# Kernel optimization log

Hardware: AMD Instinct MI355X
Metric: run time of the kernel (lower is better)

The kernel has to match this reference:

```python
import jax, jax.numpy as jnp
import numpy as np

HIDDEN = 1024
HEADS = 16
HEAD_DIM = HIDDEN // HEADS


def setup_inputs() -> dict:
    key = jax.random.key(0)
    ks = jax.random.split(key, 7)
    B, S = 2, 2048
    scale = 1.0 / np.sqrt(HIDDEN)
    return {
        "hidden_states": jax.random.normal(ks[0], (B, S, HIDDEN), dtype=jnp.float32),
        "attention_mask": jnp.zeros((B, S), dtype=jnp.float32),
        "Wq": jax.random.normal(ks[1], (HIDDEN, HIDDEN), dtype=jnp.float32) * scale,
        "bq": jnp.zeros((HIDDEN,), dtype=jnp.float32),
        "Wk": jax.random.normal(ks[2], (HIDDEN, HIDDEN), dtype=jnp.float32) * scale,
        "bk": jnp.zeros((HIDDEN,), dtype=jnp.float32),
        "Wv": jax.random.normal(ks[3], (HIDDEN, HIDDEN), dtype=jnp.float32) * scale,
        "bv": jnp.zeros((HIDDEN,), dtype=jnp.float32),
    }


def reference(hidden_states, attention_mask, Wq, bq, Wk, bk, Wv, bv):
    B, S, _ = hidden_states.shape
    def heads(x):  # [B,S,HIDDEN] -> [B,H,S,D]
        return x.reshape(B, S, HEADS, HEAD_DIM).transpose(0, 2, 1, 3)
    q = heads(hidden_states @ Wq + bq)
    k = heads(hidden_states @ Wk + bk)
    v = heads(hidden_states @ Wv + bv)
    scores = jnp.einsum('bhqd,bhkd->bhqk', q, k) / np.sqrt(HEAD_DIM).astype(np.float32)
    # additive mask broadcast [B,1,1,S]
    scores = scores + attention_mask[:, None, None, :]
    probs = jax.nn.softmax(scores, axis=-1)
    # dropout is identity in eval mode (reference baseline)
    ctx = jnp.einsum('bhqk,bhkd->bhqd', probs, v)
    return ctx.transpose(0, 2, 1, 3).reshape(B, S, HIDDEN)
```

## Files before the change

kernel.cpp:

```cpp
#include <hip/hip_runtime.h>
#include <cstdint>
#include <cstddef>

typedef __bf16 bf16;
typedef _Float16 f16;
typedef __attribute__((ext_vector_type(8))) __bf16 bf16x8;
typedef __attribute__((ext_vector_type(4))) float f32x4;
typedef __attribute__((ext_vector_type(16))) float f32x16;
typedef __attribute__((ext_vector_type(4))) _Float16 f16x4;
typedef __attribute__((ext_vector_type(8))) _Float16 f16x8;

#define MFMA16(a, b, c) __builtin_amdgcn_mfma_f32_16x16x32_bf16((a), (b), (c), 0, 0, 0)
#define MFMA32(a, b, c) __builtin_amdgcn_mfma_f32_32x32x16_bf16((a), (b), (c), 0, 0, 0)

static constexpr int BB   = 2;
static constexpr int SS   = 2048;
static constexpr int HID  = 1024;
static constexpr int NH   = 16;
static constexpr int HD   = 64;
static constexpr int MROW = BB * SS;
static constexpr int NQKV = 3 * HID;
static constexpr float LOG2E = 1.4426950408889634f;
static constexpr float MSHIFT = 16.0f;

__device__ __forceinline__ int SW(int r) { return ((r ^ (r >> 3)) & 7) << 4; }

__device__ __forceinline__ uint32_t pack_bf16(float a, float b) {
    union { bf16 h[2]; uint32_t u; } x;
    x.h[0] = (bf16)a; x.h[1] = (bf16)b;
    return x.u;
}

__device__ __forceinline__ uint32_t pack_raw(bf16 a, bf16 b) {
    union { bf16 h[2]; uint32_t u; } x;
    x.h[0] = a; x.h[1] = b;
    return x.u;
}

__device__ __forceinline__ float exp2i(float x) {
    float r; asm("v_exp_f32 %0, %1" : "=v"(r) : "v"(x)); return r;
}

__device__ __forceinline__ void plswap(uint32_t& a, uint32_t& b) {
    asm("v_permlane32_swap_b32 %0, %1" : "+v"(a), "+v"(b));
}

__device__ __forceinline__ void gload16(const void* g, void* l) {
    __builtin_amdgcn_global_load_lds(
        (const __attribute__((address_space(1))) void*)g,
        (__attribute__((address_space(3))) void*)l, 16, 0, 0);
}

__global__ __launch_bounds__(256) void cvt_hidden(const float* __restrict__ in,
                                                  bf16* __restrict__ out) {
    const int i = (blockIdx.x * 256 + threadIdx.x) * 8;
    float4 f0 = *(const float4*)&in[i];
    float4 f1 = *(const float4*)&in[i + 4];
    bf16x8 o;
    o[0] = (bf16)f0.x; o[1] = (bf16)f0.y; o[2] = (bf16)f0.z; o[3] = (bf16)f0.w;
    o[4] = (bf16)f1.x; o[5] = (bf16)f1.y; o[6] = (bf16)f1.z; o[7] = (bf16)f1.w;
    *(bf16x8*)&out[i] = o;
}

__global__ __launch_bounds__(256) void maskcvt(const float* __restrict__ m,
                                               float* __restrict__ o) {
    const int i = blockIdx.x * 256 + threadIdx.x;
    o[i] = m[i] * LOG2E - MSHIFT;
}

__global__ __launch_bounds__(256) void wtrans(const float* __restrict__ Wq,
                                              const float* __restrict__ Wk,
                                              const float* __restrict__ Wv,
                                              bf16* __restrict__ Wt) {
    __shared__ float tile[32][33];
    const float* W = (blockIdx.z == 0) ? Wq : (blockIdx.z == 1) ? Wk : Wv;
    bf16* O = Wt + (size_t)blockIdx.z * HID * HID;
    const int x  = blockIdx.x * 32 + threadIdx.x;
    const int y0 = blockIdx.y * 32;
#pragma unroll
    for (int i = threadIdx.y; i < 32; i += 8)
        tile[i][threadIdx.x] = W[(size_t)(y0 + i) * HID + x];
    __syncthreads();
    const int k = y0 + threadIdx.x;
#pragma unroll
    for (int i = threadIdx.y; i < 32; i += 8)
        O[(size_t)(blockIdx.x * 32 + i) * HID + k] = (bf16)tile[threadIdx.x][i];
}

__global__ __launch_bounds__(256) void qkv_gemm(
    const bf16* __restrict__ A, const bf16* __restrict__ Bt,
    const float* __restrict__ bq, const float* __restrict__ bk,
    const float* __restrict__ bv,
    bf16* __restrict__ Qo, bf16* __restrict__ Ko, bf16* __restrict__ Vo) {
    __shared__ __align__(16) bf16 As[128 * 32];
    __shared__ __align__(16) bf16 Bs[128 * 32];
    const int t = threadIdx.x, l = t & 63;
    const int l15 = l & 15, l4 = l >> 4;
    const int w = t >> 6;
    const int wm = w >> 1, wn = w & 1;
    const int m0 = blockIdx.y * 128, n0 = blockIdx.x * 128;

    f32x4 acc[4][4] = {};

    for (int kt = 0; kt < 32; ++kt) {
        const int k0 = kt * 32;
        __syncthreads();
#pragma unroll
        for (int cc = 0; cc < 2; ++cc) {
            const int c = t + cc * 256;
            const int row = c >> 2, col = (c & 3) * 8;
            gload16(&A[(size_t)(m0 + row) * HID + k0 + col], (char*)As + c * 16);
            gload16(&Bt[(size_t)(n0 + row) * HID + k0 + col], (char*)Bs + c * 16);
        }
        __syncthreads();

        bf16x8 af[4], bf_[4];
#pragma unroll
        for (int mi = 0; mi < 4; ++mi) {
            const int r = wm * 64 + mi * 16 + l15;
            af[mi] = *(const bf16x8*)((const char*)As + r * 64 + l4 * 16);
        }
#pragma unroll
        for (int ni = 0; ni < 4; ++ni) {
            const int r = wn * 64 + ni * 16 + l15;
            bf_[ni] = *(const bf16x8*)((const char*)Bs + r * 64 + l4 * 16);
        }
        __builtin_amdgcn_s_setprio(1);
#pragma unroll
        for (int mi = 0; mi < 4; ++mi)
#pragma unroll
            for (int ni = 0; ni < 4; ++ni)
                acc[mi][ni] = MFMA16(af[mi], bf_[ni], acc[mi][ni]);
        __builtin_amdgcn_s_setprio(0);
    }

#pragma unroll
    for (int mi = 0; mi < 4; ++mi) {
#pragma unroll
        for (int ni = 0; ni < 4; ++ni) {
            const int ng = n0 + wn * 64 + ni * 16 + l15;
            const int qkv = ng >> 10;
            const int nn = ng & 1023;
            const int hh = nn >> 6, dd = nn & 63;
            const float* bp = (qkv == 0) ? bq : (qkv == 1) ? bk : bv;
            bf16* op = (qkv == 0) ? Qo : (qkv == 1) ? Ko : Vo;
            const float bias = bp[nn];
            const float scl = (qkv == 0) ? 0.125f * LOG2E : 1.0f;
            const int mg = m0 + wm * 64 + mi * 16 + l4 * 4;
            const int bb = mg >> 11, ss = mg & 2047;
            bf16* dst = op + ((size_t)(bb * NH + hh) * SS + ss) * HD + dd;
#pragma unroll
            for (int j = 0; j < 4; ++j)
                dst[(size_t)j * HD] = (bf16)((acc[mi][ni][j] + bias) * scl);
        }
    }
}

__global__ __launch_bounds__(256) void attn_fwd(
    const bf16* __restrict__ Q, const bf16* __restrict__ K,
    const bf16* __restrict__ V, const float* __restrict__ mkl,
    f16* __restrict__ Op, float* __restrict__ ml) {
    __shared__ __align__(16) char Ks0[64 * 128];
    __shared__ __align__(16) char Ks1[64 * 128];
    __shared__ __align__(16) char Vt0[64 * 128];
    __shared__ __align__(16) char Vt1[64 * 128];

    const int t = threadIdx.x, l = t & 63, w = t >> 6;
    const int l31 = l & 31, h = l >> 5;

    const int bid = blockIdx.x;
    const int nid = (bid & 7) * 128 + (bid >> 3);
    const int bh = nid >> 5, kh = (nid >> 4) & 1, qb = nid & 15;
    const int q0 = qb * 128 + w * 32;
    const int kbase = kh * (SS / 2);

    const bf16* Qp = Q + (size_t)bh * SS * HD;
    const bf16* Kp = K + (size_t)bh * SS * HD;
    const bf16* Vp = V + (size_t)bh * SS * HD;
    const float* mkp = mkl + (bh >> 4) * SS;

    bf16x8 qf[4];
#pragma unroll
    for (int c = 0; c < 4; ++c)
        qf[c] = *(const bf16x8*)&Qp[(size_t)(q0 + l31) * HD + c * 16 + h * 8];

    bf16x8 ones;
#pragma unroll
    for (int i = 0; i < 8; ++i) ones[i] = (bf16)1.0f;

    f32x16 o0 = {}, o1 = {};
    f32x16 o2 = {};

    const int vp_ = t >> 3, vdb = (t & 7) * 8;

    auto stageK = [&](int tile, char* dst) {
        const int key0 = kbase + tile * 64;
#pragma unroll
        for (int cc = 0; cc < 2; ++cc) {
            const int c = t + cc * 256;
            const int row = c >> 3;
            const int csw = (c & 7) ^ ((row ^ (row >> 3)) & 7);
            gload16(&Kp[(size_t)(key0 + row) * HD + csw * 8], dst + c * 16);
        }
    };
    auto loadV = [&](int tile, bf16x8& va, bf16x8& vb) {
        const int key0 = kbase + tile * 64;
        va = *(const bf16x8*)&Vp[(size_t)(key0 + 2 * vp_) * HD + vdb];
        vb = *(const bf16x8*)&Vp[(size_t)(key0 + 2 * vp_ + 1) * HD + vdb];
    };
    auto storeV = [&](char* Vtn, const bf16x8& va, const bf16x8& vb) {
#pragma unroll
        for (int i = 0; i < 8; ++i) {
            const int d = vdb + i;
            *(uint32_t*)(Vtn + d * 128 + ((vp_ * 4) ^ SW(d))) =
                pack_raw(va[i], vb[i]);
        }
    };

    stageK(0, Ks0);
    {
        bf16x8 va, vb;
        loadV(0, va, vb);
        storeV(Vt0, va, vb);
    }
    __syncthreads();

    constexpr int NT = (SS / 2) / 64;
#pragma unroll 1
    for (int kt = 0; kt < NT; ++kt) {
        char* Ks = (kt & 1) ? Ks1 : Ks0;
        char* Vt = (kt & 1) ? Vt1 : Vt0;
        char* Ksn = (kt & 1) ? Ks0 : Ks1;
        char* Vtn = (kt & 1) ? Vt0 : Vt1;
        const int key0 = kbase + kt * 64;
        const bool more = (kt + 1) < NT;

        bf16x8 va = {}, vb = {};
        if (more) {
            stageK(kt + 1, Ksn);
            loadV(kt + 1, va, vb);
        }

        f32x16 s0, s1;
#pragma unroll
        for (int rq = 0; rq < 4; ++rq) {
            const f32x4 m0v = *(const f32x4*)&mkp[key0 + rq * 8 + 4 * h];
            const f32x4 m1v = *(const f32x4*)&mkp[key0 + 32 + rq * 8 + 4 * h];
#pragma unroll
            for (int j = 0; j < 4; ++j) {
                s0[rq * 4 + j] = m0v[j];
                s1[rq * 4 + j] = m1v[j];
            }
        }
        __builtin_amdgcn_s_setprio(1);
#pragma unroll
        for (int c = 0; c < 4; ++c) {
            const int r0 = l31;
            bf16x8 kf0 = *(const bf16x8*)(Ks + r0 * 128 +
                                          ((c * 32 + h * 16) ^ SW(r0)));
            s0 = MFMA32(kf0, qf[c], s0);
        }
#pragma unroll
        for (int c = 0; c < 4; ++c) {
            const int r1 = 32 + l31;
            bf16x8 kf1 = *(const bf16x8*)(Ks + r1 * 128 +
                                          ((c * 32 + h * 16) ^ SW(r1)));
            s1 = MFMA32(kf1, qf[c], s1);
        }
        __builtin_amdgcn_s_setprio(0);

#pragma unroll
        for (int g = 0; g < 2; ++g) {
            f32x16& st = g ? s1 : s0;
#pragma unroll
            for (int r = 0; r < 16; ++r) st[r] = exp2i(st[r]);
#pragma unroll
            for (int cc = 0; cc < 2; ++cc) {
                uint32_t wA = pack_bf16(st[8 * cc + 0], st[8 * cc + 1]);
                uint32_t wB = pack_bf16(st[8 * cc + 2], st[8 * cc + 3]);
                uint32_t wC = pack_bf16(st[8 * cc + 4], st[8 * cc + 5]);
                uint32_t wD = pack_bf16(st[8 * cc + 6], st[8 * cc + 7]);
                plswap(wA, wC);
                plswap(wB, wD);
                union { uint32_t u[4]; bf16x8 v; } pb;
                pb.u[0] = wA; pb.u[1] = wB; pb.u[2] = wC; pb.u[3] = wD;
                const int colb = g * 64 + cc * 32 + h * 16;
                __builtin_amdgcn_s_setprio(1);
                {
                    o2 = MFMA32(ones, pb.v, o2);
                    bf16x8 vf0 = *(const bf16x8*)(Vt + l31 * 128 +
                                                  (colb ^ SW(l31)));
                    o0 = MFMA32(vf0, pb.v, o0);
                    const int r1 = 32 + l31;
                    bf16x8 vf1 = *(const bf16x8*)(Vt + r1 * 128 +
                                                  (colb ^ SW(r1)));
                    o1 = MFMA32(vf1, pb.v, o1);
                }
                __builtin_amdgcn_s_setprio(0);
            }
            if (g == 0 && more) storeV(Vtn, va, vb);
        }
        __syncthreads();
    }

    const int part = kh * 512 + bh * 16 + qb;
    f16* Ob = Op + (size_t)part * 8192;
    const int row = w * 32 + l31;
#pragma unroll
    for (int rq = 0; rq < 4; ++rq) {
        f16x4 a, b2;
#pragma unroll
        for (int j = 0; j < 4; ++j) {
            a[j]  = (f16)o0[rq * 4 + j];
            b2[j] = (f16)o1[rq * 4 + j];
        }
        *(f16x4*)&Ob[row * 64 + rq * 8 + 4 * h] = a;
        *(f16x4*)&Ob[row * 64 + 32 + rq * 8 + 4 * h] = b2;
    }
    if (l < 32) ml[(size_t)part * 128 + (w * 32 + l)] = o2[0];
}

__global__ __launch_bounds__(256) void combine(
    const f16* __restrict__ Op, const float* __restrict__ ml,
    float* __restrict__ out) {
    const int tid = blockIdx.x * 256 + threadIdx.x;
    const int dg = tid & 7, gq = tid >> 3;
    const int bh = gq >> 11, s = gq & 2047;
    const int qb = s >> 7, q = s & 127;
    const int p0 = bh * 16 + qb, p1 = 512 + p0;

    const float l1 = ml[(size_t)p0 * 128 + q];
    const float l2 = ml[(size_t)p1 * 128 + q];
    const float inv = 1.0f / (l1 + l2);

    const f16x8 O1 = *(const f16x8*)&Op[(size_t)p0 * 8192 + q * 64 + dg * 8];
    const f16x8 O2 = *(const f16x8*)&Op[(size_t)p1 * 8192 + q * 64 + dg * 8];
    f32x4 r0, r1;
#pragma unroll
    for (int i = 0; i < 4; ++i) {
        r0[i] = ((float)O1[i] + (float)O2[i]) * inv;
        r1[i] = ((float)O1[4 + i] + (float)O2[4 + i]) * inv;
    }

    const int b = bh >> 4, hh = bh & 15;
    float* op = &out[((size_t)(b * SS + s)) * HID + hh * HD + dg * 8];
    *(f32x4*)op = r0;
    *(f32x4*)(op + 4) = r1;
}

extern "C" void kernel_launch(void* const* d_in, const int* in_sizes, int n_in,
                              void* d_out, int out_size, void* d_ws, size_t ws_size,
                              hipStream_t stream) {
    (void)in_sizes; (void)n_in; (void)out_size; (void)ws_size;
    const float* hs  = (const float*)d_in[0];
    const float* msk = (const float*)d_in[1];
    const float* Wq  = (const float*)d_in[2];
    const float* bq  = (const float*)d_in[3];
    const float* Wk  = (const float*)d_in[4];
    const float* bk  = (const float*)d_in[5];
    const float* Wv  = (const float*)d_in[6];
    const float* bv  = (const float*)d_in[7];
    float* out = (float*)d_out;
    char* ws = (char*)d_ws;
    const size_t MB = 1 << 20;

    bf16* Qb  = (bf16*)ws;
    bf16* Kb  = (bf16*)(ws + 8 * MB);
    bf16* Vb  = (bf16*)(ws + 16 * MB);
    float* mk2 = (float*)(ws + 24 * MB);
    bf16* Xb  = (bf16*)(ws + 25 * MB);
    bf16* Wt  = (bf16*)(ws + 33 * MB);
    f16* Opp  = (f16*)(ws + 25 * MB);
    float* mlp = (float*)(ws + 59 * MB);

    cvt_hidden<<<dim3(MROW * HID / (256 * 8)), dim3(256), 0, stream>>>(hs, Xb);
    maskcvt<<<dim3(BB * SS / 256), dim3(256), 0, stream>>>(msk, mk2);
    wtrans<<<dim3(32, 32, 3), dim3(32, 8), 0, stream>>>(Wq, Wk, Wv, Wt);
    qkv_gemm<<<dim3(NQKV / 128, MROW / 128), dim3(256), 0, stream>>>(
        Xb, Wt, bq, bk, bv, Qb, Kb, Vb);
    attn_fwd<<<dim3(1024), dim3(256), 0, stream>>>(Qb, Kb, Vb, mk2, Opp, mlp);
    combine<<<dim3(2048), dim3(256), 0, stream>>>(Opp, mlp, out);
}
```

Before: 120.1 us.

## Split attention keys four ways and compute row sums on VALU

The attention kernel now splits the key range into four partitions instead of two, doubling the grid to 2048 blocks with half as many key tiles each. The combine kernel now sums four partial outputs and four row-sum partials. The softmax denominator is no longer computed by an extra MFMA against a vector of ones; each lane accumulates exp values in fp32 and a cross-half shuffle finishes the row sum. This trades more partial-output traffic and combine work for better parallel balance and fewer matrix instructions, and the denominator now uses unrounded fp32 probabilities while the PV product uses bf16-rounded ones.

```diff
diff --git a/kernel.cpp b/kernel.cpp
--- a/kernel.cpp
+++ b/kernel.cpp
@@ -169,10 +169,10 @@
     const int l31 = l & 31, h = l >> 5;
 
     const int bid = blockIdx.x;
-    const int nid = (bid & 7) * 128 + (bid >> 3);
-    const int bh = nid >> 5, kh = (nid >> 4) & 1, qb = nid & 15;
+    const int nid = (bid & 7) * 256 + (bid >> 3);
+    const int bh = nid >> 6, kh = (nid >> 4) & 3, qb = nid & 15;
     const int q0 = qb * 128 + w * 32;
-    const int kbase = kh * (SS / 2);
+    const int kbase = kh * (SS / 4);
 
     const bf16* Qp = Q + (size_t)bh * SS * HD;
     const bf16* Kp = K + (size_t)bh * SS * HD;
@@ -184,12 +184,8 @@
     for (int c = 0; c < 4; ++c)
         qf[c] = *(const bf16x8*)&Qp[(size_t)(q0 + l31) * HD + c * 16 + h * 8];
 
-    bf16x8 ones;
-#pragma unroll
-    for (int i = 0; i < 8; ++i) ones[i] = (bf16)1.0f;
-
+    float lrun = 0.f;
     f32x16 o0 = {}, o1 = {};
-    f32x16 o2 = {};
 
     const int vp_ = t >> 3, vdb = (t & 7) * 8;
 
@@ -225,7 +221,7 @@
     }
     __syncthreads();
 
-    constexpr int NT = (SS / 2) / 64;
+    constexpr int NT = (SS / 4) / 64;
 #pragma unroll 1
     for (int kt = 0; kt < NT; ++kt) {
         char* Ks = (kt & 1) ? Ks1 : Ks0;
@@ -272,8 +268,14 @@
 #pragma unroll
         for (int g = 0; g < 2; ++g) {
             f32x16& st = g ? s1 : s0;
-#pragma unroll
-            for (int r = 0; r < 16; ++r) st[r] = exp2i(st[r]);
+            float ps = 0.f;
+#pragma unroll
+            for (int r = 0; r < 16; ++r) {
+                const float p = exp2i(st[r]);
+                st[r] = p;
+                ps += p;
+            }
+            lrun += ps;
 #pragma unroll
             for (int cc = 0; cc < 2; ++cc) {
                 uint32_t wA = pack_bf16(st[8 * cc + 0], st[8 * cc + 1]);
@@ -287,7 +289,6 @@
                 const int colb = g * 64 + cc * 32 + h * 16;
                 __builtin_amdgcn_s_setprio(1);
                 {
-                    o2 = MFMA32(ones, pb.v, o2);
                     bf16x8 vf0 = *(const bf16x8*)(Vt + l31 * 128 +
                                                   (colb ^ SW(l31)));
                     o0 = MFMA32(vf0, pb.v, o0);
@@ -303,6 +304,7 @@
         __syncthreads();
     }
 
+    lrun += __shfl_xor(lrun, 32);
     const int part = kh * 512 + bh * 16 + qb;
     f16* Ob = Op + (size_t)part * 8192;
     const int row = w * 32 + l31;
@@ -317,7 +319,7 @@
         *(f16x4*)&Ob[row * 64 + rq * 8 + 4 * h] = a;
         *(f16x4*)&Ob[row * 64 + 32 + rq * 8 + 4 * h] = b2;
     }
-    if (l < 32) ml[(size_t)part * 128 + (w * 32 + l)] = o2[0];
+    if (l < 32) ml[(size_t)part * 128 + (w * 32 + l)] = lrun;
 }
 
 __global__ __launch_bounds__(256) void combine(
@@ -327,20 +329,24 @@
     const int dg = tid & 7, gq = tid >> 3;
     const int bh = gq >> 11, s = gq & 2047;
     const int qb = s >> 7, q = s & 127;
-    const int p0 = bh * 16 + qb, p1 = 512 + p0;
-
-    const float l1 = ml[(size_t)p0 * 128 + q];
-    const float l2 = ml[(size_t)p1 * 128 + q];
-    const float inv = 1.0f / (l1 + l2);
-
-    const f16x8 O1 = *(const f16x8*)&Op[(size_t)p0 * 8192 + q * 64 + dg * 8];
-    const f16x8 O2 = *(const f16x8*)&Op[(size_t)p1 * 8192 + q * 64 + dg * 8];
+    const int pb = bh * 16 + qb;
+
+    float lsum = 0.f;
+#pragma unroll
+    for (int i = 0; i < 4; ++i) lsum += ml[(size_t)(i * 512 + pb) * 128 + q];
+    const float inv = 1.0f / lsum;
+
+    float acc[8] = {};
+#pragma unroll
+    for (int i = 0; i < 4; ++i) {
+        const f16x8 O = *(const f16x8*)&Op[(size_t)(i * 512 + pb) * 8192 +
+                                           q * 64 + dg * 8];
+#pragma unroll
+        for (int j = 0; j < 8; ++j) acc[j] += (float)O[j];
+    }
     f32x4 r0, r1;
 #pragma unroll
-    for (int i = 0; i < 4; ++i) {
-        r0[i] = ((float)O1[i] + (float)O2[i]) * inv;
-        r1[i] = ((float)O1[4 + i] + (float)O2[4 + i]) * inv;
-    }
+    for (int i = 0; i < 4; ++i) { r0[i] = acc[i] * inv; r1[i] = acc[4 + i] * inv; }
 
     const int b = bh >> 4, hh = bh & 15;
     float* op = &out[((size_t)(b * SS + s)) * HID + hh * HD + dg * 8];
@@ -378,6 +384,6 @@
     wtrans<<<dim3(32, 32, 3), dim3(32, 8), 0, stream>>>(Wq, Wk, Wv, Wt);
     qkv_gemm<<<dim3(NQKV / 128, MROW / 128), dim3(256), 0, stream>>>(
         Xb, Wt, bq, bk, bv, Qb, Kb, Vb);
-    attn_fwd<<<dim3(1024), dim3(256), 0, stream>>>(Qb, Kb, Vb, mk2, Opp, mlp);
+    attn_fwd<<<dim3(2048), dim3(256), 0, stream>>>(Qb, Kb, Vb, mk2, Opp, mlp);
     combine<<<dim3(2048), dim3(256), 0, stream>>>(Opp, mlp, out);
 }
```

New measurement: 121.5 us. No clear change (+1.2%).

## Store V transposed from QKV GEMM and compute softmax row sums in VALU

Applied to the files above, without the earlier changes.

The QKV projection epilogue now writes V in a [B,H,D,S] transposed layout, so the attention kernel can stage V tiles straight into LDS with async global-to-LDS loads instead of loading into registers and scattering a transposed copy. The row-sum of probabilities is now accumulated with scalar adds plus a cross-half shuffle, replacing the extra MFMA against a ones vector. This removes per-tile register transposes and one of three MFMAs in the PV loop. In exchange the GEMM epilogue writes V with a strided, less coalesced pattern, and the sum now uses fp32 probabilities rather than the bf16-rounded ones fed to the MFMA.

```diff
diff --git a/kernel.cpp b/kernel.cpp
--- a/kernel.cpp
+++ b/kernel.cpp
@@ -9,6 +9,7 @@
 typedef __attribute__((ext_vector_type(16))) float f32x16;
 typedef __attribute__((ext_vector_type(4))) _Float16 f16x4;
 typedef __attribute__((ext_vector_type(8))) _Float16 f16x8;
+typedef __attribute__((ext_vector_type(4))) short short4v;
 
 #define MFMA16(a, b, c) __builtin_amdgcn_mfma_f32_16x16x32_bf16((a), (b), (c), 0, 0, 0)
 #define MFMA32(a, b, c) __builtin_amdgcn_mfma_f32_32x32x16_bf16((a), (b), (c), 0, 0, 0)
@@ -28,12 +29,6 @@
 __device__ __forceinline__ uint32_t pack_bf16(float a, float b) {
     union { bf16 h[2]; uint32_t u; } x;
     x.h[0] = (bf16)a; x.h[1] = (bf16)b;
-    return x.u;
-}
-
-__device__ __forceinline__ uint32_t pack_raw(bf16 a, bf16 b) {
-    union { bf16 h[2]; uint32_t u; } x;
-    x.h[0] = a; x.h[1] = b;
     return x.u;
 }
 
@@ -142,23 +137,33 @@
             const int qkv = ng >> 10;
             const int nn = ng & 1023;
             const int hh = nn >> 6, dd = nn & 63;
-            const float* bp = (qkv == 0) ? bq : (qkv == 1) ? bk : bv;
-            bf16* op = (qkv == 0) ? Qo : (qkv == 1) ? Ko : Vo;
-            const float bias = bp[nn];
-            const float scl = (qkv == 0) ? 0.125f * LOG2E : 1.0f;
             const int mg = m0 + wm * 64 + mi * 16 + l4 * 4;
             const int bb = mg >> 11, ss = mg & 2047;
-            bf16* dst = op + ((size_t)(bb * NH + hh) * SS + ss) * HD + dd;
-#pragma unroll
-            for (int j = 0; j < 4; ++j)
-                dst[(size_t)j * HD] = (bf16)((acc[mi][ni][j] + bias) * scl);
+            if (qkv == 2) {
+                const float bias = bv[nn];
+                union { bf16 h[4]; short4v s4; } pk_;
+#pragma unroll
+                for (int j = 0; j < 4; ++j)
+                    pk_.h[j] = (bf16)(acc[mi][ni][j] + bias);
+                bf16* dst = Vo + ((size_t)(bb * NH + hh) * HD + dd) * SS + ss;
+                *(short4v*)dst = pk_.s4;
+            } else {
+                const float* bp = (qkv == 0) ? bq : bk;
+                bf16* op = (qkv == 0) ? Qo : Ko;
+                const float bias = bp[nn];
+                const float scl = (qkv == 0) ? 0.125f * LOG2E : 1.0f;
+                bf16* dst = op + ((size_t)(bb * NH + hh) * SS + ss) * HD + dd;
+#pragma unroll
+                for (int j = 0; j < 4; ++j)
+                    dst[(size_t)j * HD] = (bf16)((acc[mi][ni][j] + bias) * scl);
+            }
         }
     }
 }
 
 __global__ __launch_bounds__(256) void attn_fwd(
     const bf16* __restrict__ Q, const bf16* __restrict__ K,
-    const bf16* __restrict__ V, const float* __restrict__ mkl,
+    const bf16* __restrict__ Vt_g, const float* __restrict__ mkl,
     f16* __restrict__ Op, float* __restrict__ ml) {
     __shared__ __align__(16) char Ks0[64 * 128];
     __shared__ __align__(16) char Ks1[64 * 128];
@@ -174,9 +179,9 @@
     const int q0 = qb * 128 + w * 32;
     const int kbase = kh * (SS / 2);
 
-    const bf16* Qp = Q + (size_t)bh * SS * HD;
-    const bf16* Kp = K + (size_t)bh * SS * HD;
-    const bf16* Vp = V + (size_t)bh * SS * HD;
+    const bf16* Qp  = Q + (size_t)bh * SS * HD;
+    const bf16* Kp  = K + (size_t)bh * SS * HD;
+    const bf16* Vpt = Vt_g + (size_t)bh * HD * SS;
     const float* mkp = mkl + (bh >> 4) * SS;
 
     bf16x8 qf[4];
@@ -184,14 +189,8 @@
     for (int c = 0; c < 4; ++c)
         qf[c] = *(const bf16x8*)&Qp[(size_t)(q0 + l31) * HD + c * 16 + h * 8];
 
-    bf16x8 ones;
-#pragma unroll
-    for (int i = 0; i < 8; ++i) ones[i] = (bf16)1.0f;
-
+    float lrun = 0.f;
     f32x16 o0 = {}, o1 = {};
-    f32x16 o2 = {};
-
-    const int vp_ = t >> 3, vdb = (t & 7) * 8;
 
     auto stageK = [&](int tile, char* dst) {
         const int key0 = kbase + tile * 64;
@@ -203,26 +202,19 @@
             gload16(&Kp[(size_t)(key0 + row) * HD + csw * 8], dst + c * 16);
         }
     };
-    auto loadV = [&](int tile, bf16x8& va, bf16x8& vb) {
+    auto stageVt = [&](int tile, char* dst) {
         const int key0 = kbase + tile * 64;
-        va = *(const bf16x8*)&Vp[(size_t)(key0 + 2 * vp_) * HD + vdb];
-        vb = *(const bf16x8*)&Vp[(size_t)(key0 + 2 * vp_ + 1) * HD + vdb];
+#pragma unroll
+        for (int cc = 0; cc < 2; ++cc) {
+            const int c = t + cc * 256;
+            const int row = c >> 3;
+            const int csw = (c & 7) ^ ((row ^ (row >> 3)) & 7);
+            gload16(&Vpt[(size_t)row * SS + key0 + csw * 8], dst + c * 16);
+        }
     };
-    auto storeV = [&](char* Vtn, const bf16x8& va, const bf16x8& vb) {
-#pragma unroll
-        for (int i = 0; i < 8; ++i) {
-            const int d = vdb + i;
-            *(uint32_t*)(Vtn + d * 128 + ((vp_ * 4) ^ SW(d))) =
-                pack_raw(va[i], vb[i]);
-        }
-    };
 
     stageK(0, Ks0);
-    {
-        bf16x8 va, vb;
-        loadV(0, va, vb);
-        storeV(Vt0, va, vb);
-    }
+    stageVt(0, Vt0);
     __syncthreads();
 
     constexpr int NT = (SS / 2) / 64;
@@ -235,10 +227,9 @@
         const int key0 = kbase + kt * 64;
         const bool more = (kt + 1) < NT;
 
-        bf16x8 va = {}, vb = {};
         if (more) {
             stageK(kt + 1, Ksn);
-            loadV(kt + 1, va, vb);
+            stageVt(kt + 1, Vtn);
         }
 
         f32x16 s0, s1;
@@ -272,8 +263,14 @@
 #pragma unroll
         for (int g = 0; g < 2; ++g) {
             f32x16& st = g ? s1 : s0;
-#pragma unroll
-            for (int r = 0; r < 16; ++r) st[r] = exp2i(st[r]);
+            float ps = 0.f;
+#pragma unroll
+            for (int r = 0; r < 16; ++r) {
+                const float p = exp2i(st[r]);
+                st[r] = p;
+                ps += p;
+            }
+            lrun += ps;
 #pragma unroll
             for (int cc = 0; cc < 2; ++cc) {
                 uint32_t wA = pack_bf16(st[8 * cc + 0], st[8 * cc + 1]);
@@ -287,7 +284,6 @@
                 const int colb = g * 64 + cc * 32 + h * 16;
                 __builtin_amdgcn_s_setprio(1);
                 {
-                    o2 = MFMA32(ones, pb.v, o2);
                     bf16x8 vf0 = *(const bf16x8*)(Vt + l31 * 128 +
                                                   (colb ^ SW(l31)));
                     o0 = MFMA32(vf0, pb.v, o0);
@@ -298,11 +294,11 @@
                 }
                 __builtin_amdgcn_s_setprio(0);
             }
-            if (g == 0 && more) storeV(Vtn, va, vb);
         }
         __syncthreads();
     }
 
+    lrun += __shfl_xor(lrun, 32);
     const int part = kh * 512 + bh * 16 + qb;
     f16* Ob = Op + (size_t)part * 8192;
     const int row = w * 32 + l31;
@@ -317,7 +313,7 @@
         *(f16x4*)&Ob[row * 64 + rq * 8 + 4 * h] = a;
         *(f16x4*)&Ob[row * 64 + 32 + rq * 8 + 4 * h] = b2;
     }
-    if (l < 32) ml[(size_t)part * 128 + (w * 32 + l)] = o2[0];
+    if (l < 32) ml[(size_t)part * 128 + (w * 32 + l)] = lrun;
 }
 
 __global__ __launch_bounds__(256) void combine(
```

Measured after the change: 119.6 us. No clear change (-0.4%).
